# Kernel tuning notes

Hardware: AMD Instinct MI355X
Metric: run time of the kernel (lower is better)

## Reference

```python
import jax, jax.numpy as jnp
import numpy as np

NUM_EXPERTS = 8
TOP_K = 2
N_EMBD = 1024
FF_HIDDEN = 4096


def setup_inputs() -> dict:
    key = jax.random.key(0)
    ks = jax.random.split(key, 5)
    scale = 0.02
    inputs = jax.random.normal(ks[0], (4, 2048, N_EMBD), dtype=jnp.float32)
    # torch Linear weights: (out_features, in_features)
    wg = jax.random.normal(ks[1], (NUM_EXPERTS, N_EMBD), dtype=jnp.float32) * scale
    w1 = jax.random.normal(ks[2], (NUM_EXPERTS, FF_HIDDEN, N_EMBD), dtype=jnp.float32) * scale
    w2 = jax.random.normal(ks[3], (NUM_EXPERTS, N_EMBD, FF_HIDDEN), dtype=jnp.float32) * scale
    w3 = jax.random.normal(ks[4], (NUM_EXPERTS, FF_HIDDEN, N_EMBD), dtype=jnp.float32) * scale
    return {"inputs": inputs, "wg": wg, "w1": w1, "w2": w2, "w3": w3}


def reference(inputs, wg, w1, w2, w3):
    B, S, D = inputs.shape
    xs = inputs.reshape(-1, D)                      # [T, D]
    T = xs.shape[0]
    E = wg.shape[0]
    gate_logits = xs @ wg.T                          # [T, E]
    top_w, sel = jax.lax.top_k(gate_logits, TOP_K)   # [T, K]
    top_w = jax.nn.softmax(top_w.astype(jnp.float32), axis=-1).astype(inputs.dtype)
    # scatter top-k weights into dense per-expert combine weights [T, E]
    combine = jnp.zeros((T, E), dtype=inputs.dtype)
    combine = combine.at[jnp.arange(T)[:, None], sel].set(top_w)
    out = jnp.zeros_like(xs)
    for e in range(E):  # small fixed loop over experts (structurally distinct weights)
        h = jax.nn.silu(xs @ w1[e].T) * (xs @ w3[e].T)   # [T, H]
        out = out + combine[:, e:e + 1] * (h @ w2[e].T)  # [T, D]
    return out.reshape(B, S, D)
```

## Files before the change

### kernel.cpp

```cpp
#include <hip/hip_runtime.h>
#include <math.h>

#define NEXP 8
#define TTOK 8192
#define DEMB 1024
#define HFF  4096

#define OFF_CNT   0
#define OFF_OFFS  64
#define OFF_PTOK  1024
#define OFF_PW    (OFF_PTOK + NEXP*TTOK*4)
#define OFF_XB    (OFF_PW + NEXP*TTOK*4)
#define OFF_HB    (OFF_XB + TTOK*DEMB*2)

typedef short bf16x8 __attribute__((ext_vector_type(8)));
typedef float f32x4 __attribute__((ext_vector_type(4)));

__device__ __forceinline__ unsigned short f2bf(float f) {
  union { float f; unsigned int u; } v; v.f = f;
  unsigned int r = v.u + 0x7fffu + ((v.u >> 16) & 1u);
  return (unsigned short)(r >> 16);
}

__device__ __forceinline__ void pack4(float4 v, void* dst) {
  uint2 r;
  r.x = (unsigned)f2bf(v.x) | ((unsigned)f2bf(v.y) << 16);
  r.y = (unsigned)f2bf(v.z) | ((unsigned)f2bf(v.w) << 16);
  *(uint2*)dst = r;
}

__device__ __forceinline__ void gll16(const void* g, void* l) {
  __builtin_amdgcn_global_load_lds(
      (const __attribute__((address_space(1))) unsigned int*)g,
      (__attribute__((address_space(3))) unsigned int*)l, 16, 0, 0);
}

__global__ void k_convert_x(const float* __restrict__ x, ushort4* __restrict__ xb) {
  int i = blockIdx.x * 256 + threadIdx.x;
  float4 v = ((const float4*)x)[i];
  ushort4 o;
  o.x = f2bf(v.x); o.y = f2bf(v.y); o.z = f2bf(v.z); o.w = f2bf(v.w);
  xb[i] = o;
}

__global__ __launch_bounds__(256) void k_gate(
    const float* __restrict__ x, const float* __restrict__ wg,
    int* __restrict__ cnt, int* __restrict__ ptok, float* __restrict__ pw) {
  __shared__ float wgs[NEXP * DEMB];
  int tid = threadIdx.x;
  for (int i = tid; i < NEXP * DEMB / 4; i += 256)
    ((float4*)wgs)[i] = ((const float4*)wg)[i];
  __syncthreads();
  int lane = tid & 63;
  int t = blockIdx.x * 4 + (tid >> 6);
  const float* xr = x + (size_t)t * DEMB;
  float acc[NEXP];
#pragma unroll
  for (int e = 0; e < NEXP; ++e) acc[e] = 0.f;
#pragma unroll
  for (int j = 0; j < DEMB / 64; ++j) {
    int d = lane + j * 64;
    float xv = xr[d];
#pragma unroll
    for (int e = 0; e < NEXP; ++e) acc[e] += xv * wgs[e * DEMB + d];
  }
#pragma unroll
  for (int e = 0; e < NEXP; ++e) {
#pragma unroll
    for (int off = 32; off > 0; off >>= 1) acc[e] += __shfl_xor(acc[e], off);
  }
  if (lane == 0) {
    float b0 = -1e30f; int i0 = 0;
#pragma unroll
    for (int e = 0; e < NEXP; ++e) if (acc[e] > b0) { b0 = acc[e]; i0 = e; }
    float b1 = -1e30f; int i1 = 0;
#pragma unroll
    for (int e = 0; e < NEXP; ++e) if (e != i0 && acc[e] > b1) { b1 = acc[e]; i1 = e; }
    float ex = expf(b1 - b0);
    float s  = 1.f + ex;
    float w0 = 1.f / s;
    float w1v = ex / s;
    int s0 = atomicAdd(&cnt[i0], 1);
    ptok[i0 * TTOK + s0] = t; pw[i0 * TTOK + s0] = w0;
    int s1 = atomicAdd(&cnt[i1], 1);
    ptok[i1 * TTOK + s1] = t; pw[i1 * TTOK + s1] = w1v;
  }
}

__global__ void k_scan(const int* __restrict__ cnt, int* __restrict__ offs) {
  if (threadIdx.x == 0) {
    int s = 0;
    for (int e = 0; e < NEXP; ++e) { offs[e] = s; s += cnt[e]; }
  }
}


__global__ __launch_bounds__(256, 2) void k_gemm1(
    const unsigned short* __restrict__ Xb, const float* __restrict__ w1,
    const float* __restrict__ w3, const int* __restrict__ cnt,
    const int* __restrict__ offs, const int* __restrict__ ptok,
    unsigned short* __restrict__ Hb, int e_sel, int mbase, int mTiles) {
  int nwg = gridDim.x;
  int orig = blockIdx.x;
  int idp = (orig & 7) * (nwg >> 3) + (orig >> 3);
  int mt, e, nt;
  if (e_sel >= 0) { e = e_sel; mt = idp % mTiles; nt = idp / mTiles; }
  else { mt = idp % mTiles; e = (idp / mTiles) % NEXP; nt = idp / (mTiles * NEXP); }
  int ce = cnt[e];
  int m0 = mbase + mt * 128;
  if (m0 >= ce) return;
  int n0 = nt * 128;
  int hb = (e_sel >= 0) ? -mbase : offs[e];

  __shared__ __align__(16) unsigned char sm[49152];
  unsigned char* As = sm;
  unsigned char* B1 = sm + 16384;
  unsigned char* B3 = sm + 32768;

  int tid = threadIdx.x, lane = tid & 63, wid = tid >> 6;
  int wm = (wid >> 1) * 64, wn = (wid & 1) * 64;
  const float* w1e = w1 + (size_t)e * HFF * DEMB;
  const float* w3e = w3 + (size_t)e * HFF * DEMB;

  const unsigned short* asrcb[4];
#pragma unroll
  for (int it = 0; it < 4; ++it) {
    int c = it * 256 + tid;
    int row = c >> 3;
    int slot = m0 + row; slot = slot < ce ? slot : ce - 1;
    int tok = ptok[e * TTOK + slot];
    asrcb[it] = Xb + (size_t)tok * DEMB + (size_t)(((c & 7) ^ (row & 7)) * 8);
  }

  const f32x4 zf = {0.f, 0.f, 0.f, 0.f};
  f32x4 au[4][4], av[4][4];
#pragma unroll
  for (int a = 0; a < 4; ++a)
#pragma unroll
    for (int b = 0; b < 4; ++b) { au[a][b] = zf; av[a][b] = zf; }

  for (int kt = 0; kt < DEMB / 64; ++kt) {
    int k0 = kt * 64;
#pragma unroll
    for (int it = 0; it < 4; ++it)
      gll16(asrcb[it] + k0, As + it * 4096 + wid * 1024);
#pragma unroll
    for (int i = 0; i < 8; ++i) {
      int idx = i * 256 + tid;
      int n = idx >> 4, f4 = idx & 15;
      int bb = n * 128 + (((f4 >> 1) ^ (n & 7)) * 16) + (f4 & 1) * 8;
      size_t goff = (size_t)(n0 + n) * DEMB + k0 + f4 * 4;
      pack4(*(const float4*)(w1e + goff), B1 + bb);
      pack4(*(const float4*)(w3e + goff), B3 + bb);
    }
    __syncthreads();
#pragma unroll
    for (int kk = 0; kk < 64; kk += 32) {
      bf16x8 af[4], b1f[4], b3f[4];
      int kg = (kk >> 3) + (lane >> 4);
#pragma unroll
      for (int mr = 0; mr < 4; ++mr) {
        int r = wm + mr * 16 + (lane & 15);
        af[mr] = *(const bf16x8*)(As + r * 128 + ((kg ^ (r & 7)) * 16));
      }
#pragma unroll
      for (int nr = 0; nr < 4; ++nr) {
        int c = wn + nr * 16 + (lane & 15);
        int boff = c * 128 + ((kg ^ (c & 7)) * 16);
        b1f[nr] = *(const bf16x8*)(B1 + boff);
        b3f[nr] = *(const bf16x8*)(B3 + boff);
      }
#pragma unroll
      for (int mr = 0; mr < 4; ++mr)
#pragma unroll
        for (int nr = 0; nr < 4; ++nr) {
          au[mr][nr] = __builtin_amdgcn_mfma_f32_16x16x32_bf16(af[mr], b1f[nr], au[mr][nr], 0, 0, 0);
          av[mr][nr] = __builtin_amdgcn_mfma_f32_16x16x32_bf16(af[mr], b3f[nr], av[mr][nr], 0, 0, 0);
        }
    }
    __syncthreads();
  }
#pragma unroll
  for (int mr = 0; mr < 4; ++mr) {
#pragma unroll
    for (int j = 0; j < 4; ++j) {
      int rs = m0 + wm + mr * 16 + (lane >> 4) * 4 + j;
      if (rs < ce) {
        unsigned short* hrow = Hb + (size_t)(hb + rs) * HFF + n0 + wn + (lane & 15);
#pragma unroll
        for (int nr = 0; nr < 4; ++nr) {
          float u = au[mr][nr][j], v = av[mr][nr][j];
          float h = v * (u / (1.f + __expf(-u)));
          hrow[nr * 16] = f2bf(h);
        }
      }
    }
  }
}

__global__ __launch_bounds__(256, 2) void k_gemm2(
    const unsigned short* __restrict__ Hb, const float* __restrict__ w2,
    const int* __restrict__ cnt, const int* __restrict__ offs,
    const int* __restrict__ ptok, const float* __restrict__ pw,
    float* __restrict__ out, int e_sel, int mbase, int mTiles) {
  int nwg = gridDim.x;
  int orig = blockIdx.x;
  int idp = (orig & 7) * (nwg >> 3) + (orig >> 3);
  int mt, e, nt;
  if (e_sel >= 0) { e = e_sel; mt = idp % mTiles; nt = idp / mTiles; }
  else { mt = idp % mTiles; e = (idp / mTiles) % NEXP; nt = idp / (mTiles * NEXP); }
  int ce = cnt[e];
  int m0 = mbase + mt * 128;
  if (m0 >= ce) return;
  int n0 = nt * 128;
  int hb = (e_sel >= 0) ? -mbase : offs[e];

  __shared__ __align__(16) unsigned char sm[32768];
  unsigned char* As = sm;
  unsigned char* B2 = sm + 16384;

  int tid = threadIdx.x, lane = tid & 63, wid = tid >> 6;
  int wm = (wid >> 1) * 64, wn = (wid & 1) * 64;
  const float* w2e = w2 + (size_t)e * DEMB * HFF;

  const unsigned short* asrcb[4];
#pragma unroll
  for (int it = 0; it < 4; ++it) {
    int c = it * 256 + tid;
    int row = c >> 3;
    int slot = m0 + row; slot = slot < ce ? slot : ce - 1;
    asrcb[it] = Hb + (size_t)(hb + slot) * HFF + (size_t)(((c & 7) ^ (row & 7)) * 8);
  }

  const f32x4 zf = {0.f, 0.f, 0.f, 0.f};
  f32x4 acc[4][4];
#pragma unroll
  for (int a = 0; a < 4; ++a)
#pragma unroll
    for (int b = 0; b < 4; ++b) acc[a][b] = zf;

  for (int kt = 0; kt < HFF / 64; ++kt) {
    int k0 = kt * 64;
#pragma unroll
    for (int it = 0; it < 4; ++it)
      gll16(asrcb[it] + k0, As + it * 4096 + wid * 1024);
#pragma unroll
    for (int i = 0; i < 8; ++i) {
      int idx = i * 256 + tid;
      int n = idx >> 4, f4 = idx & 15;
      pack4(*(const float4*)(w2e + (size_t)(n0 + n) * HFF + k0 + f4 * 4),
            B2 + n * 128 + (((f4 >> 1) ^ (n & 7)) * 16) + (f4 & 1) * 8);
    }
    __syncthreads();
#pragma unroll
    for (int kk = 0; kk < 64; kk += 32) {
      bf16x8 af[4], bf_[4];
      int kg = (kk >> 3) + (lane >> 4);
#pragma unroll
      for (int mr = 0; mr < 4; ++mr) {
        int r = wm + mr * 16 + (lane & 15);
        af[mr] = *(const bf16x8*)(As + r * 128 + ((kg ^ (r & 7)) * 16));
      }
#pragma unroll
      for (int nr = 0; nr < 4; ++nr) {
        int c = wn + nr * 16 + (lane & 15);
        bf_[nr] = *(const bf16x8*)(B2 + c * 128 + ((kg ^ (c & 7)) * 16));
      }
#pragma unroll
      for (int mr = 0; mr < 4; ++mr)
#pragma unroll
        for (int nr = 0; nr < 4; ++nr)
          acc[mr][nr] = __builtin_amdgcn_mfma_f32_16x16x32_bf16(af[mr], bf_[nr], acc[mr][nr], 0, 0, 0);
    }
    __syncthreads();
  }
#pragma unroll
  for (int mr = 0; mr < 4; ++mr) {
#pragma unroll
    for (int j = 0; j < 4; ++j) {
      int rs = m0 + wm + mr * 16 + (lane >> 4) * 4 + j;
      if (rs < ce) {
        int tok = ptok[e * TTOK + rs];
        float gw = pw[e * TTOK + rs];
        float* orow = out + (size_t)tok * DEMB + n0 + wn + (lane & 15);
#pragma unroll
        for (int nr = 0; nr < 4; ++nr)
          atomicAdd(orow + nr * 16, acc[mr][nr][j] * gw);
      }
    }
  }
}

extern "C" void kernel_launch(void* const* d_in, const int* in_sizes, int n_in,
                              void* d_out, int out_size, void* d_ws, size_t ws_size,
                              hipStream_t stream) {
  const float* x  = (const float*)d_in[0];
  const float* wg = (const float*)d_in[1];
  const float* w1 = (const float*)d_in[2];
  const float* w2 = (const float*)d_in[3];
  const float* w3 = (const float*)d_in[4];
  char* ws = (char*)d_ws;
  int*   cnt  = (int*)(ws + OFF_CNT);
  int*   offs = (int*)(ws + OFF_OFFS);
  int*   ptok = (int*)(ws + OFF_PTOK);
  float* pw   = (float*)(ws + OFF_PW);
  unsigned short* Xb = (unsigned short*)(ws + OFF_XB);
  unsigned short* Hb = (unsigned short*)(ws + OFF_HB);
  float* out = (float*)d_out;

  hipMemsetAsync(ws + OFF_CNT, 0, 256, stream);
  hipMemsetAsync(d_out, 0, (size_t)out_size * sizeof(float), stream);
  k_convert_x<<<TTOK * DEMB / 4 / 256, 256, 0, stream>>>(x, (ushort4*)Xb);
  k_gate<<<TTOK / 4, 256, 0, stream>>>(x, wg, cnt, ptok, pw);
  k_scan<<<1, 64, 0, stream>>>(cnt, offs);

  long long hbRows = ((long long)ws_size - OFF_HB) / (HFF * 2);
  if (hbRows >= 2LL * TTOK) {
    k_gemm1<<<NEXP * 64 * 32, 256, 0, stream>>>(Xb, w1, w3, cnt, offs, ptok, Hb, -1, 0, 64);
    k_gemm2<<<NEXP * 64 * 8, 256, 0, stream>>>(Hb, w2, cnt, offs, ptok, pw, out, -1, 0, 64);
  } else {
    int chunkTiles = (int)(hbRows / 128);
    if (chunkTiles < 1) chunkTiles = 1;
    if (chunkTiles > 64) chunkTiles = 64;
    for (int e = 0; e < NEXP; ++e) {
      for (int mb = 0; mb < TTOK; mb += chunkTiles * 128) {
        int mT = chunkTiles;
        if (mb + mT * 128 > TTOK) mT = (TTOK - mb) / 128;
        k_gemm1<<<mT * 32, 256, 0, stream>>>(Xb, w1, w3, cnt, offs, ptok, Hb, e, mb, mT);
        k_gemm2<<<mT * 8, 256, 0, stream>>>(Hb, w2, cnt, offs, ptok, pw, out, e, mb, mT);
      }
    }
  }
}
```

Baseline: 1.294 ms.

## Pre-convert expert weights to bf16 and load them directly into LDS

Adds a kernel that converts w1, w3 and w2 to bf16 in workspace once per call. The GEMM kernels then fetch weight tiles with global_load_lds instead of loading fp32 and packing in registers inside the loop. The x-to-bf16 conversion is fused into the gating kernel. This removes redundant per-tile fp32 weight traffic and conversion ALU work, at the cost of an extra full pass over the weights and more workspace.

```diff
diff --git a/kernel.cpp b/kernel.cpp
--- a/kernel.cpp
+++ b/kernel.cpp
@@ -11,7 +11,7 @@
 #define OFF_PTOK  1024
 #define OFF_PW    (OFF_PTOK + NEXP*TTOK*4)
 #define OFF_XB    (OFF_PW + NEXP*TTOK*4)
-#define OFF_HB    (OFF_XB + TTOK*DEMB*2)
+#define OFF_WB    (OFF_XB + (size_t)TTOK*DEMB*2)
 
 typedef short bf16x8 __attribute__((ext_vector_type(8)));
 typedef float f32x4 __attribute__((ext_vector_type(4)));
@@ -22,30 +22,28 @@
   return (unsigned short)(r >> 16);
 }
 
-__device__ __forceinline__ void pack4(float4 v, void* dst) {
-  uint2 r;
-  r.x = (unsigned)f2bf(v.x) | ((unsigned)f2bf(v.y) << 16);
-  r.y = (unsigned)f2bf(v.z) | ((unsigned)f2bf(v.w) << 16);
-  *(uint2*)dst = r;
-}
-
 __device__ __forceinline__ void gll16(const void* g, void* l) {
   __builtin_amdgcn_global_load_lds(
       (const __attribute__((address_space(1))) unsigned int*)g,
       (__attribute__((address_space(3))) unsigned int*)l, 16, 0, 0);
 }
 
-__global__ void k_convert_x(const float* __restrict__ x, ushort4* __restrict__ xb) {
-  int i = blockIdx.x * 256 + threadIdx.x;
-  float4 v = ((const float4*)x)[i];
-  ushort4 o;
-  o.x = f2bf(v.x); o.y = f2bf(v.y); o.z = f2bf(v.z); o.w = f2bf(v.w);
-  xb[i] = o;
+__global__ void k_convert_w(const float* __restrict__ w, uint4* __restrict__ wb) {
+  size_t i = (size_t)blockIdx.x * 256 + threadIdx.x;
+  float4 a = ((const float4*)w)[2 * i];
+  float4 b = ((const float4*)w)[2 * i + 1];
+  uint4 o;
+  o.x = (unsigned)f2bf(a.x) | ((unsigned)f2bf(a.y) << 16);
+  o.y = (unsigned)f2bf(a.z) | ((unsigned)f2bf(a.w) << 16);
+  o.z = (unsigned)f2bf(b.x) | ((unsigned)f2bf(b.y) << 16);
+  o.w = (unsigned)f2bf(b.z) | ((unsigned)f2bf(b.w) << 16);
+  wb[i] = o;
 }
 
 __global__ __launch_bounds__(256) void k_gate(
     const float* __restrict__ x, const float* __restrict__ wg,
-    int* __restrict__ cnt, int* __restrict__ ptok, float* __restrict__ pw) {
+    int* __restrict__ cnt, int* __restrict__ ptok, float* __restrict__ pw,
+    unsigned short* __restrict__ xb) {
   __shared__ float wgs[NEXP * DEMB];
   int tid = threadIdx.x;
   for (int i = tid; i < NEXP * DEMB / 4; i += 256)
@@ -54,15 +52,22 @@
   int lane = tid & 63;
   int t = blockIdx.x * 4 + (tid >> 6);
   const float* xr = x + (size_t)t * DEMB;
+  unsigned short* xbr = xb + (size_t)t * DEMB;
   float acc[NEXP];
 #pragma unroll
   for (int e = 0; e < NEXP; ++e) acc[e] = 0.f;
 #pragma unroll
-  for (int j = 0; j < DEMB / 64; ++j) {
-    int d = lane + j * 64;
-    float xv = xr[d];
-#pragma unroll
-    for (int e = 0; e < NEXP; ++e) acc[e] += xv * wgs[e * DEMB + d];
+  for (int j = 0; j < 4; ++j) {
+    int d = j * 256 + lane * 4;
+    float4 v = *(const float4*)(xr + d);
+    ushort4 o;
+    o.x = f2bf(v.x); o.y = f2bf(v.y); o.z = f2bf(v.z); o.w = f2bf(v.w);
+    *(ushort4*)(xbr + d) = o;
+#pragma unroll
+    for (int e = 0; e < NEXP; ++e) {
+      float4 w = *(const float4*)(wgs + e * DEMB + d);
+      acc[e] += v.x * w.x + v.y * w.y + v.z * w.z + v.w * w.w;
+    }
   }
 #pragma unroll
   for (int e = 0; e < NEXP; ++e) {
@@ -96,8 +101,8 @@
 
 
 __global__ __launch_bounds__(256, 2) void k_gemm1(
-    const unsigned short* __restrict__ Xb, const float* __restrict__ w1,
-    const float* __restrict__ w3, const int* __restrict__ cnt,
+    const unsigned short* __restrict__ Xb, const unsigned short* __restrict__ w1b,
+    const unsigned short* __restrict__ w3b, const int* __restrict__ cnt,
     const int* __restrict__ offs, const int* __restrict__ ptok,
     unsigned short* __restrict__ Hb, int e_sel, int mbase, int mTiles) {
   int nwg = gridDim.x;
@@ -111,6 +116,9 @@
   if (m0 >= ce) return;
   int n0 = nt * 128;
   int hb = (e_sel >= 0) ? -mbase : offs[e];
+  size_t eo = (size_t)((e_sel >= 0) ? 0 : e) * HFF * DEMB;
+  const unsigned short* w1e = w1b + eo;
+  const unsigned short* w3e = w3b + eo;
 
   __shared__ __align__(16) unsigned char sm[49152];
   unsigned char* As = sm;
@@ -119,17 +127,18 @@
 
   int tid = threadIdx.x, lane = tid & 63, wid = tid >> 6;
   int wm = (wid >> 1) * 64, wn = (wid & 1) * 64;
-  const float* w1e = w1 + (size_t)e * HFF * DEMB;
-  const float* w3e = w3 + (size_t)e * HFF * DEMB;
-
-  const unsigned short* asrcb[4];
+
+  const unsigned short *as[4], *b1s[4], *b3s[4];
 #pragma unroll
   for (int it = 0; it < 4; ++it) {
     int c = it * 256 + tid;
     int row = c >> 3;
+    int col = ((c & 7) ^ (row & 7)) * 8;
     int slot = m0 + row; slot = slot < ce ? slot : ce - 1;
     int tok = ptok[e * TTOK + slot];
-    asrcb[it] = Xb + (size_t)tok * DEMB + (size_t)(((c & 7) ^ (row & 7)) * 8);
+    as[it]  = Xb + (size_t)tok * DEMB + col;
+    b1s[it] = w1e + (size_t)(n0 + row) * DEMB + col;
+    b3s[it] = w3e + (size_t)(n0 + row) * DEMB + col;
   }
 
   const f32x4 zf = {0.f, 0.f, 0.f, 0.f};
@@ -142,17 +151,11 @@
   for (int kt = 0; kt < DEMB / 64; ++kt) {
     int k0 = kt * 64;
 #pragma unroll
-    for (int it = 0; it < 4; ++it)
-      gll16(asrcb[it] + k0, As + it * 4096 + wid * 1024);
-#pragma unroll
-    for (int i = 0; i < 8; ++i) {
-      int idx = i * 256 + tid;
-      int n = idx >> 4, f4 = idx & 15;
-      int bb = n * 128 + (((f4 >> 1) ^ (n & 7)) * 16) + (f4 & 1) * 8;
-      size_t goff = (size_t)(n0 + n) * DEMB + k0 + f4 * 4;
-      pack4(*(const float4*)(w1e + goff), B1 + bb);
-      pack4(*(const float4*)(w3e + goff), B3 + bb);
-    }
+    for (int it = 0; it < 4; ++it) gll16(as[it] + k0,  As + it * 4096 + wid * 1024);
+#pragma unroll
+    for (int it = 0; it < 4; ++it) gll16(b1s[it] + k0, B1 + it * 4096 + wid * 1024);
+#pragma unroll
+    for (int it = 0; it < 4; ++it) gll16(b3s[it] + k0, B3 + it * 4096 + wid * 1024);
     __syncthreads();
 #pragma unroll
     for (int kk = 0; kk < 64; kk += 32) {
@@ -199,7 +202,7 @@
 }
 
 __global__ __launch_bounds__(256, 2) void k_gemm2(
-    const unsigned short* __restrict__ Hb, const float* __restrict__ w2,
+    const unsigned short* __restrict__ Hb, const unsigned short* __restrict__ w2b,
     const int* __restrict__ cnt, const int* __restrict__ offs,
     const int* __restrict__ ptok, const float* __restrict__ pw,
     float* __restrict__ out, int e_sel, int mbase, int mTiles) {
@@ -214,6 +217,8 @@
   if (m0 >= ce) return;
   int n0 = nt * 128;
   int hb = (e_sel >= 0) ? -mbase : offs[e];
+  size_t eo = (size_t)((e_sel >= 0) ? 0 : e) * DEMB * HFF;
+  const unsigned short* w2e = w2b + eo;
 
   __shared__ __align__(16) unsigned char sm[32768];
   unsigned char* As = sm;
@@ -221,15 +226,16 @@
 
   int tid = threadIdx.x, lane = tid & 63, wid = tid >> 6;
   int wm = (wid >> 1) * 64, wn = (wid & 1) * 64;
-  const float* w2e = w2 + (size_t)e * DEMB * HFF;
-
-  const unsigned short* asrcb[4];
+
+  const unsigned short *as[4], *b2s[4];
 #pragma unroll
   for (int it = 0; it < 4; ++it) {
     int c = it * 256 + tid;
     int row = c >> 3;
+    int col = ((c & 7) ^ (row & 7)) * 8;
     int slot = m0 + row; slot = slot < ce ? slot : ce - 1;
-    asrcb[it] = Hb + (size_t)(hb + slot) * HFF + (size_t)(((c & 7) ^ (row & 7)) * 8);
+    as[it]  = Hb + (size_t)(hb + slot) * HFF + col;
+    b2s[it] = w2e + (size_t)(n0 + row) * HFF + col;
   }
 
   const f32x4 zf = {0.f, 0.f, 0.f, 0.f};
@@ -242,15 +248,9 @@
   for (int kt = 0; kt < HFF / 64; ++kt) {
     int k0 = kt * 64;
 #pragma unroll
-    for (int it = 0; it < 4; ++it)
-      gll16(asrcb[it] + k0, As + it * 4096 + wid * 1024);
-#pragma unroll
-    for (int i = 0; i < 8; ++i) {
-      int idx = i * 256 + tid;
-      int n = idx >> 4, f4 = idx & 15;
-      pack4(*(const float4*)(w2e + (size_t)(n0 + n) * HFF + k0 + f4 * 4),
-            B2 + n * 128 + (((f4 >> 1) ^ (n & 7)) * 16) + (f4 & 1) * 8);
-    }
+    for (int it = 0; it < 4; ++it) gll16(as[it] + k0,  As + it * 4096 + wid * 1024);
+#pragma unroll
+    for (int it = 0; it < 4; ++it) gll16(b2s[it] + k0, B2 + it * 4096 + wid * 1024);
     __syncthreads();
 #pragma unroll
     for (int kk = 0; kk < 64; kk += 32) {
@@ -305,30 +305,48 @@
   int*   ptok = (int*)(ws + OFF_PTOK);
   float* pw   = (float*)(ws + OFF_PW);
   unsigned short* Xb = (unsigned short*)(ws + OFF_XB);
-  unsigned short* Hb = (unsigned short*)(ws + OFF_HB);
   float* out = (float*)d_out;
 
+  const size_t WPE = (size_t)HFF * DEMB;
   hipMemsetAsync(ws + OFF_CNT, 0, 256, stream);
   hipMemsetAsync(d_out, 0, (size_t)out_size * sizeof(float), stream);
-  k_convert_x<<<TTOK * DEMB / 4 / 256, 256, 0, stream>>>(x, (ushort4*)Xb);
-  k_gate<<<TTOK / 4, 256, 0, stream>>>(x, wg, cnt, ptok, pw);
+  k_gate<<<TTOK / 4, 256, 0, stream>>>(x, wg, cnt, ptok, pw, Xb);
   k_scan<<<1, 64, 0, stream>>>(cnt, offs);
 
-  long long hbRows = ((long long)ws_size - OFF_HB) / (HFF * 2);
-  if (hbRows >= 2LL * TTOK) {
-    k_gemm1<<<NEXP * 64 * 32, 256, 0, stream>>>(Xb, w1, w3, cnt, offs, ptok, Hb, -1, 0, 64);
-    k_gemm2<<<NEXP * 64 * 8, 256, 0, stream>>>(Hb, w2, cnt, offs, ptok, pw, out, -1, 0, 64);
+  size_t needA = OFF_WB + 3 * NEXP * WPE * 2 + (size_t)2 * TTOK * HFF * 2;
+  if (ws_size >= needA) {
+    unsigned short* w1b = (unsigned short*)(ws + OFF_WB);
+    unsigned short* w3b = w1b + NEXP * WPE;
+    unsigned short* w2b = w3b + NEXP * WPE;
+    unsigned short* Hb  = w2b + NEXP * WPE;
+    int cgrid = (int)(NEXP * WPE / 8 / 256);
+    k_convert_w<<<cgrid, 256, 0, stream>>>(w1, (uint4*)w1b);
+    k_convert_w<<<cgrid, 256, 0, stream>>>(w3, (uint4*)w3b);
+    k_convert_w<<<cgrid, 256, 0, stream>>>(w2, (uint4*)w2b);
+    k_gemm1<<<NEXP * 64 * 32, 256, 0, stream>>>(Xb, w1b, w3b, cnt, offs, ptok, Hb, -1, 0, 64);
+    k_gemm2<<<NEXP * 64 * 8, 256, 0, stream>>>(Hb, w2b, cnt, offs, ptok, pw, out, -1, 0, 64);
   } else {
+    unsigned short* w1b = (unsigned short*)(ws + OFF_WB);
+    unsigned short* w3b = w1b + WPE;
+    unsigned short* w2b = w3b + WPE;
+    unsigned short* Hb  = w2b + WPE;
+    size_t offHbC = OFF_WB + 3 * WPE * 2;
+    long long hbRows = ((long long)ws_size - (long long)offHbC) / (HFF * 2);
     int chunkTiles = (int)(hbRows / 128);
     if (chunkTiles < 1) chunkTiles = 1;
     if (chunkTiles > 64) chunkTiles = 64;
+    int cgrid = (int)(WPE / 8 / 256);
     for (int e = 0; e < NEXP; ++e) {
+      k_convert_w<<<cgrid, 256, 0, stream>>>(w1 + e * WPE, (uint4*)w1b);
+      k_convert_w<<<cgrid, 256, 0, stream>>>(w3 + e * WPE, (uint4*)w3b);
+      k_convert_w<<<cgrid, 256, 0, stream>>>(w2 + e * WPE, (uint4*)w2b);
       for (int mb = 0; mb < TTOK; mb += chunkTiles * 128) {
         int mT = chunkTiles;
         if (mb + mT * 128 > TTOK) mT = (TTOK - mb) / 128;
-        k_gemm1<<<mT * 32, 256, 0, stream>>>(Xb, w1, w3, cnt, offs, ptok, Hb, e, mb, mT);
-        k_gemm2<<<mT * 8, 256, 0, stream>>>(Hb, w2, cnt, offs, ptok, pw, out, e, mb, mT);
-      }
-    }
-  }
-}
+        if (mT < 1) break;
+        k_gemm1<<<mT * 32, 256, 0, stream>>>(Xb, w1b, w3b, cnt, offs, ptok, Hb, e, mb, mT);
+        k_gemm2<<<mT * 8, 256, 0, stream>>>(Hb, w2b, cnt, offs, ptok, pw, out, e, mb, mT);
+      }
+    }
+  }
+}
```

After: 1.135 ms. 1.14x faster.
